# Kernel optimization log

Hardware: AMD Instinct MI355X
Metric: run time of the kernel (lower is better)

Reference implementation:

```python
import jax, jax.numpy as jnp
import numpy as np

DN = ('NCHW', 'OIHW', 'NCHW')
SCALES = (4, 2, 5, 2, 1914)  # per-feature one-hot widths; sum=1927, +1 scalar row = 1928 CNN channels


def conv(x, w, b, stride):
    y = jax.lax.conv_general_dilated(x, w, stride, 'VALID', dimension_numbers=DN)
    return y + b[None, :, None, None]


def maxpool(x, window):
    return jax.lax.reduce_window(x, -jnp.inf, jax.lax.max, (1, 1) + window, (1, 1) + window, 'VALID')


def setup_inputs() -> dict:
    key = jax.random.key(0)
    ks = jax.random.split(key, 16)
    B, T, F, H, W = 2, 32, 8, 128, 128
    replay = jax.random.randint(ks[0], (B, T, F, H, W), 0, 2).astype(jnp.float32)

    def rn(k, shape, scale=0.02):
        return jax.random.normal(k, shape, jnp.float32) * scale

    return dict(
        replay_tensor=replay,
        emb_table=rn(ks[1], (16384, 200), 1.0),
        conv_con_w=rn(ks[2], (1, 1, 4, 4)), conv_con_b=jnp.zeros((1,), jnp.float32),
        fc_con_w=rn(ks[3], (200, 961)), fc_con_b=jnp.zeros((200,), jnp.float32),
        cnn1_w=rn(ks[4], (964, 1928, 1, 2)), cnn1_b=jnp.zeros((964,), jnp.float32),
        cnn2_w=rn(ks[5], (482, 964, 1, 2)), cnn2_b=jnp.zeros((482,), jnp.float32),
        cnn3_w=rn(ks[6], (241, 482, 1, 2)), cnn3_b=jnp.zeros((241,), jnp.float32),
        cnn4_w=rn(ks[7], (100, 241, 1, 2)), cnn4_b=jnp.zeros((100,), jnp.float32),
        fc_cnn_w=rn(ks[8], (100, 2300)), fc_cnn_b=jnp.zeros((100,), jnp.float32),
        lstm_w_ih=rn(ks[9], (400, 100), 0.1), lstm_w_hh=rn(ks[10], (400, 100), 0.1),
        lstm_b_ih=jnp.zeros((400,), jnp.float32), lstm_b_hh=jnp.zeros((400,), jnp.float32),
        fc_out_w=rn(ks[11], (2, 100), 0.1), fc_out_b=jnp.zeros((2,), jnp.float32),
        batch_size=2,
    )


def reference(replay_tensor, emb_table, conv_con_w, conv_con_b, fc_con_w, fc_con_b,
              cnn1_w, cnn1_b, cnn2_w, cnn2_b, cnn3_w, cnn3_b, cnn4_w, cnn4_b,
              fc_cnn_w, fc_cnn_b, lstm_w_ih, lstm_w_hh, lstm_b_ih, lstm_b_hh,
              fc_out_w, fc_out_b, batch_size):
    # np.delete(replay, 2, 2) then np.delete(., 3, 2) removes original features 2 and 4
    replay = replay_tensor[:batch_size, :, jnp.array([0, 1, 3, 5, 6, 7])]
    B, T = replay.shape[0], replay.shape[1]
    scalar = replay[:, :, 0]   # [B,T,128,128]
    cat = replay[:, :, 1:6]    # [B,T,5,128,128]

    # --- categorical branch ---
    # The original builds a [scale_k, H*W] one-hot scatter per (b,t,k), then the
    # embedding step reads only spatial column 0: row s of the per-feature block is
    # emb_table[1] iff value_at_pos0 == s (nonzero after thresholding), else emb_table[0].
    v0 = cat[:, :, :, 0, 0].astype(jnp.int32)  # [B,T,5]
    embs = []
    for k, sc in enumerate(SCALES):
        v = v0[:, :, k]
        v = jnp.where(v > sc, 0, v)  # threshold: values > scale_ zeroed
        idx = ((jnp.arange(sc)[None, None, :] == v[:, :, None]) & (v[:, :, None] != 0)).astype(jnp.int32)
        embs.append(emb_table[idx])  # [B,T,sc,200]
    emb_full = jnp.concatenate(embs, axis=2)  # [B,T,1927,200]

    # --- scalar conv branch (faithful to the bug: cnn_con2 applied to raw x) ---
    x = scalar.reshape(B * T, 1, 128, 128)
    y = maxpool(jax.nn.relu(conv(x, conv_con_w, conv_con_b, (2, 2))), (2, 2))  # [BT,1,31,31]
    y = y.reshape(B * T, -1) @ fc_con_w.T + fc_con_b                           # [BT,200]
    sca_full = y.reshape(B, T, 1, 200)

    # --- CNN over concatenated [1928, 1, 200] frames ---
    z = jnp.concatenate([sca_full, emb_full], axis=2).reshape(B * T, 1928, 1, 200)
    z = maxpool(jax.nn.relu(conv(z, cnn1_w, cnn1_b, (1, 1))), (1, 2))
    z = maxpool(jax.nn.relu(conv(z, cnn2_w, cnn2_b, (1, 1))), (1, 2))
    z = maxpool(jax.nn.relu(conv(z, cnn3_w, cnn3_b, (1, 1))), (1, 2))
    z = jax.nn.relu(conv(z, cnn4_w, cnn4_b, (1, 1)))  # [BT,100,1,23]
    z = z.reshape(B * T, -1) @ fc_cnn_w.T + fc_cnn_b  # [BT,100]
    seq = z.reshape(B, T, 100)

    # --- single-layer LSTM (torch gate order i,f,g,o), zero init state ---
    def step(carry, x_t):
        h, c = carry
        g = x_t @ lstm_w_ih.T + h @ lstm_w_hh.T + lstm_b_ih + lstm_b_hh
        i, f, gg, o = jnp.split(g, 4, axis=-1)
        c = jax.nn.sigmoid(f) * c + jax.nn.sigmoid(i) * jnp.tanh(gg)
        h = jax.nn.sigmoid(o) * jnp.tanh(c)
        return (h, c), None

    h0 = jnp.zeros((B, 100), seq.dtype)
    c0 = jnp.zeros((B, 100), seq.dtype)
    (hT, _), _ = jax.lax.scan(step, (h0, c0), jnp.swapaxes(seq, 0, 1))
    return hT @ fc_out_w.T + fc_out_b  # [B,2]
```

## Files before the change

### kernel.cpp

```cpp
#include <hip/hip_runtime.h>
#include <math.h>

#define DEVFN __device__ __forceinline__

typedef __bf16 bf16x8 __attribute__((ext_vector_type(8)));
typedef float f32x4 __attribute__((ext_vector_type(4)));

constexpr int T_ = 32;
constexpr int HW = 128;
constexpr int C1IN = 1928;
constexpr int C1 = 964;

DEVFN float sigm(float x) { return 1.0f / (1.0f + __expf(-x)); }
DEVFN float tanhfast(float x) { return 2.0f / (1.0f + __expf(-2.0f * x)) - 1.0f; }

DEVFN ushort f2b(float v) {
    union { float f; unsigned u; } x; x.f = v;
    unsigned r = x.u + 0x7fffu + ((x.u >> 16) & 1u);
    return (ushort)(r >> 16);
}

DEVFN void gload16(const ushort* g, ushort* l) {
    __builtin_amdgcn_global_load_lds(
        (const __attribute__((address_space(1))) unsigned int*)g,
        (__attribute__((address_space(3))) unsigned int*)l, 16, 0, 0);
}

__global__ void k_sca_conv(const float* __restrict__ replay, const float* __restrict__ wc,
                           const float* __restrict__ bc, float* __restrict__ y) {
    const int n = blockIdx.x;
    const int idx = blockIdx.y * 256 + threadIdx.x;
    if (idx >= 961) return;
    const float* x = replay + (size_t)n * 8 * HW * HW;
    float wr_[16];
    #pragma unroll
    for (int t = 0; t < 16; ++t) wr_[t] = wc[t];
    const float bcv = bc[0];
    const int i = idx / 31, j = idx % 31;
    float m = 0.0f;
    #pragma unroll
    for (int di = 0; di < 2; ++di)
    #pragma unroll
    for (int dj = 0; dj < 2; ++dj) {
        const int h0 = 2 * (2 * i + di), w0 = 2 * (2 * j + dj);
        float acc = bcv;
        #pragma unroll
        for (int p = 0; p < 4; ++p)
        #pragma unroll
        for (int q = 0; q < 4; ++q)
            acc += x[(h0 + p) * HW + (w0 + q)] * wr_[p * 4 + q];
        m = fmaxf(m, fmaxf(acc, 0.0f));
    }
    y[n * 961 + idx] = m;
}

__global__ void k_sca_fc(const float* __restrict__ y, const float* __restrict__ fcw,
                         const float* __restrict__ fcb, float* __restrict__ sca) {
    const int n = blockIdx.x;
    const int wid = threadIdx.x >> 6, lane = threadIdx.x & 63;
    const int o = blockIdx.y * 4 + wid;
    float acc = 0.f;
    for (int m = lane; m < 961; m += 64)
        acc += y[n * 961 + m] * fcw[(size_t)o * 961 + m];
    #pragma unroll
    for (int off = 32; off > 0; off >>= 1) acc += __shfl_down(acc, off);
    if (lane == 0) sca[n * 200 + o] = acc + fcb[o];
}

__global__ void k_prep(const float* __restrict__ w1, const float* __restrict__ w2,
                       const float* __restrict__ w3, const float* __restrict__ w4,
                       const float* __restrict__ whh, const float* __restrict__ replay,
                       float* __restrict__ wsum, float* __restrict__ sa,
                       ushort* __restrict__ A2, ushort* __restrict__ A3,
                       ushort* __restrict__ A4, float* __restrict__ whhT) {
    const int bid = blockIdx.x;
    const int tx = threadIdx.x;
    constexpr int N2 = 2 * 512 * 1024;
    constexpr int N3 = 2 * 256 * 512;
    constexpr int N4 = 2 * 128 * 256;
    if (bid < 5533) {
        const int idx = bid * 256 + tx;
        if (idx < N2) {
            const int kw = idx >> 19;
            const int r = idx & 524287;
            const int oc = r >> 10, ic = r & 1023;
            const float v = (oc < 482 && ic < 964) ? w2[(size_t)oc * 1928 + ic * 2 + kw] : 0.f;
            A2[idx] = f2b(v);
        } else if (idx < N2 + N3) {
            const int j = idx - N2;
            const int kw = j >> 17;
            const int r = j & 131071;
            const int oc = r >> 9, ic = r & 511;
            const float v = (oc < 241 && ic < 482) ? w3[(size_t)oc * 964 + ic * 2 + kw] : 0.f;
            A3[j] = f2b(v);
        } else if (idx < N2 + N3 + N4) {
            const int j = idx - (N2 + N3);
            const int kw = j >> 15;
            const int r = j & 32767;
            const int oc = r >> 8, ic = r & 255;
            const float v = (oc < 100 && ic < 241) ? w4[(size_t)oc * 482 + ic * 2 + kw] : 0.f;
            A4[j] = f2b(v);
        } else {
            const int j = idx - (N2 + N3 + N4);
            if (j < 40000) {
                const int m = j / 400, p = j - m * 400;
                const int go = (p & 3) * 100 + (p >> 2);
                whhT[m * 400 + p] = whh[go * 100 + m];
            }
        }
    } else if (bid < 5774) {
        const int oc = (bid - 5533) * 4 + (tx >> 6);
        const int lane = tx & 63;
        const float* wr = w1 + (size_t)oc * C1IN * 2;
        float s0 = 0.f, s1 = 0.f;
        for (int ic = lane; ic < C1IN; ic += 64) {
            s0 += wr[ic * 2 + 0];
            s1 += wr[ic * 2 + 1];
        }
        #pragma unroll
        for (int off = 32; off > 0; off >>= 1) {
            s0 += __shfl_down(s0, off);
            s1 += __shfl_down(s1, off);
        }
        if (lane == 0) { wsum[oc * 2] = s0; wsum[oc * 2 + 1] = s1; }
    } else {
        const int j = bid - 5774;
        const int n = j >> 2;
        const int oc = (j & 3) * 256 + tx;
        if (oc < C1) {
            const int chs[5]    = {1, 3, 5, 6, 7};
            const int scales[5] = {4, 2, 5, 2, 1914};
            const int offs[5]   = {0, 4, 6, 11, 13};
            float s0 = 0.f, s1 = 0.f;
            #pragma unroll
            for (int k = 0; k < 5; ++k) {
                int v = (int)replay[((size_t)n * 8 + chs[k]) * HW * HW];
                if (v > scales[k]) v = 0;
                if (v >= 1 && v <= scales[k] - 1) {
                    const int ic = 1 + offs[k] + v;
                    s0 += w1[((size_t)oc * C1IN + ic) * 2 + 0];
                    s1 += w1[((size_t)oc * C1IN + ic) * 2 + 1];
                }
            }
            sa[(n * C1 + oc) * 2 + 0] = s0;
            sa[(n * C1 + oc) * 2 + 1] = s1;
        }
    }
}

template <int OCT>
__global__ void k_cnn1(const float* __restrict__ sca, const float* __restrict__ emb,
                       const float* __restrict__ w1, const float* __restrict__ b1,
                       const float* __restrict__ wsum, const float* __restrict__ sa,
                       ushort* __restrict__ Bt2) {
    const int n = blockIdx.x;
    const int ocBase = blockIdx.y * OCT;
    const int tx = threadIdx.x;
    __shared__ float ev[200], sv[200], dv[200];
    __shared__ float oscal[OCT][7];
    __shared__ float vals[OCT][100];
    for (int i = tx; i < 200; i += blockDim.x) {
        const float e0 = emb[i], e1 = emb[200 + i];
        ev[i] = e0;
        dv[i] = e1 - e0;
        sv[i] = sca[n * 200 + i] - e0;
    }
    for (int i = tx; i < OCT * 7; i += blockDim.x) {
        const int ocl = i / 7, f = i % 7;
        const int oc = ocBase + ocl;
        float v = 0.f;
        if (oc < C1) {
            switch (f) {
                case 0: v = wsum[oc * 2 + 0]; break;
                case 1: v = wsum[oc * 2 + 1]; break;
                case 2: v = b1[oc]; break;
                case 3: v = w1[(size_t)oc * C1IN * 2 + 0]; break;
                case 4: v = w1[(size_t)oc * C1IN * 2 + 1]; break;
                case 5: v = sa[(n * C1 + oc) * 2 + 0]; break;
                case 6: v = sa[(n * C1 + oc) * 2 + 1]; break;
            }
        }
        oscal[ocl][f] = v;
    }
    __syncthreads();
    for (int item = tx; item < OCT * 99; item += blockDim.x) {
        const int ocl = item / 99, u = item % 99;
        const int oc = ocBase + ocl;
        float res = 0.f;
        if (oc < C1) {
            const float ws0 = oscal[ocl][0], ws1 = oscal[ocl][1], bb = oscal[ocl][2];
            const float a0 = oscal[ocl][3], a1 = oscal[ocl][4];
            const float s0 = oscal[ocl][5], s1 = oscal[ocl][6];
            float r = -INFINITY;
            #pragma unroll
            for (int dw = 0; dw < 2; ++dw) {
                const int ww = 2 * u + dw;
                const float o = bb + ws0 * ev[ww] + ws1 * ev[ww + 1]
                                   + a0 * sv[ww] + a1 * sv[ww + 1]
                                   + s0 * dv[ww] + s1 * dv[ww + 1];
                r = fmaxf(r, o);
            }
            res = fmaxf(r, 0.0f);
        }
        vals[ocl][u] = res;
    }
    __syncthreads();
    for (int i = tx; i < OCT * 100; i += blockDim.x) {
        const int u = i >> 4, ocl = i & 15;
        const float v = (u < 99) ? vals[ocl][u] : 0.0f;
        Bt2[(size_t)(n * 100 + u) * 1024 + ocBase + ocl] = f2b(v);
    }
    if (n == 0 && ocBase == 0) {
        for (int i = tx; i < 1024; i += blockDim.x)
            Bt2[(size_t)6400 * 1024 + i] = 0;
    }
}

template <int OCREAL, int WR, int WOUT, int KICP, int MPAD, int OMODE, int OSTR,
          bool POOL, int MT, int NTILES>
__global__ __launch_bounds__(256, 2) void k_gemm_conv(
    const ushort* __restrict__ A, const ushort* __restrict__ Bt,
    const float* __restrict__ bias, void* __restrict__ outv) {
    constexpr int BK = 64;
    constexpr int NT = KICP / BK;
    constexpr int NWG = MT * NTILES;
    constexpr int Qq = NWG / 8, Rr = NWG % 8;

    __shared__ __align__(16) ushort As0[2][4096];
    __shared__ __align__(16) ushort As1[2][4096];
    __shared__ __align__(16) ushort Bs[2][8704];

    const int bid = blockIdx.x;
    const int xcd = bid & 7, rest = bid >> 3;
    const int base = (xcd < Rr) ? xcd * (Qq + 1) : Rr * (Qq + 1) + (xcd - Rr) * Qq;
    const int sid = base + rest;
    const int mBase = (sid % MT) * 64;
    const int nBase = (sid / MT) * 128;

    const int tx = threadIdx.x;
    const int wave = tx >> 6, lane = tx & 63;
    const int lr = lane & 15, lk = lane >> 4;
    const int r8 = lane >> 3;
    const int cx = (lane & 7) ^ r8;
    const ushort* A1p = A + (size_t)MPAD * KICP;

    f32x4 acc[4][2] = {};

    auto STAGE = [&](int buf, int kt) {
        const int k0 = kt * BK + cx * 8;
        #pragma unroll
        for (int it = 0; it < 2; ++it) {
            const int s = wave + it * 4;
            const int row = s * 8 + r8;
            gload16(&A[(size_t)(mBase + row) * KICP + k0], &As0[buf][s * 512]);
            gload16(&A1p[(size_t)(mBase + row) * KICP + k0], &As1[buf][s * 512]);
        }
        #pragma unroll
        for (int it = 0; it < 4; ++it) {
            const int s = wave + it * 4;
            const int row = s * 8 + r8;
            gload16(&Bt[(size_t)(nBase + row) * KICP + k0], &Bs[buf][s * 512]);
        }
        if (wave == 0) {
            const int row = 128 + r8;
            gload16(&Bt[(size_t)(nBase + row) * KICP + k0], &Bs[buf][16 * 512]);
        }
    };

    auto COMPUTE = [&](int cur) {
        #pragma unroll
        for (int ks = 0; ks < 2; ++ks) {
            bf16x8 a0[4], a1[4], b0[2], b1[2];
            #pragma unroll
            for (int i = 0; i < 4; ++i) {
                const int row = i * 16 + lr;
                const int col = (ks * 32 + lk * 8) ^ ((row & 7) << 3);
                a0[i] = *(const bf16x8*)&As0[cur][row * 64 + col];
                a1[i] = *(const bf16x8*)&As1[cur][row * 64 + col];
            }
            #pragma unroll
            for (int j = 0; j < 2; ++j) {
                const int row = wave * 32 + j * 16 + lr;
                const int col = (ks * 32 + lk * 8) ^ ((row & 7) << 3);
                b0[j] = *(const bf16x8*)&Bs[cur][row * 64 + col];
                const int row1 = row + 1;
                const int col1 = (ks * 32 + lk * 8) ^ ((row1 & 7) << 3);
                b1[j] = *(const bf16x8*)&Bs[cur][row1 * 64 + col1];
            }
            #pragma unroll
            for (int i = 0; i < 4; ++i)
                #pragma unroll
                for (int j = 0; j < 2; ++j) {
                    acc[i][j] = __builtin_amdgcn_mfma_f32_16x16x32_bf16(a0[i], b0[j], acc[i][j], 0, 0, 0);
                    acc[i][j] = __builtin_amdgcn_mfma_f32_16x16x32_bf16(a1[i], b1[j], acc[i][j], 0, 0, 0);
                }
        }
    };

    STAGE(0, 0);
    if (NT > 1) STAGE(1, 1);
    #pragma unroll 1
    for (int kt = 0; kt < NT; ++kt) {
        const int cur = kt & 1;
        if (kt + 1 < NT) {
            if (wave == 0) asm volatile("s_waitcnt vmcnt(9)" ::: "memory");
            else           asm volatile("s_waitcnt vmcnt(8)" ::: "memory");
        } else {
            asm volatile("s_waitcnt vmcnt(0)" ::: "memory");
        }
        __builtin_amdgcn_sched_barrier(0);
        __builtin_amdgcn_s_barrier();
        COMPUTE(cur);
        __builtin_amdgcn_s_barrier();
        if (kt + 2 < NT) STAGE(cur, kt + 2);
    }

    ushort* outb = (ushort*)outv;
    float*  outf = (float*)outv;
    constexpr int NOUTW = POOL ? (WOUT / 2) : WOUT;
    constexpr int WRN = NOUTW + 1;
    constexpr int NVALID = WR * 64;
    #pragma unroll
    for (int i = 0; i < 4; ++i) {
        const int m0 = mBase + i * 16 + lk * 4;
        #pragma unroll
        for (int j = 0; j < 2; ++j) {
            const int r = nBase + wave * 32 + j * 16 + lr;
            const int n = r / WR, w = r - n * WR;
            #pragma unroll
            for (int reg = 0; reg < 4; ++reg) {
                const float v = acc[i][j][reg];
                const float vo = __shfl_xor(v, 1);
                const int m = m0 + reg;
                const bool lok = POOL ? ((lr & 1) == 0) : true;
                if (lok && (w < WOUT) && (m < OCREAL) && (r < NVALID)) {
                    const float pre = POOL ? fmaxf(v, vo) : v;
                    const float val = fmaxf(pre + bias[m], 0.0f);
                    const int wc = POOL ? (w >> 1) : w;
                    if (OMODE == 2)
                        outb[((size_t)(n * WRN + wc)) * OSTR + m] = f2b(val);
                    else
                        outf[((size_t)n * OCREAL + m) * NOUTW + wc] = val;
                }
            }
        }
    }
}

__global__ void k_fc_cnn(const float* __restrict__ z4, const float* __restrict__ w,
                         const float* __restrict__ b, float* __restrict__ seq) {
    const int n = blockIdx.x;
    const int wid = threadIdx.x >> 6, lane = threadIdx.x & 63;
    const int o = blockIdx.y * 4 + wid;
    const float4* zr = (const float4*)(z4 + (size_t)n * 2300);
    const float4* wr = (const float4*)(w + (size_t)o * 2300);
    float acc = 0.f;
    for (int m = lane; m < 575; m += 64) {
        const float4 wv = wr[m];
        const float4 zv = zr[m];
        acc += wv.x * zv.x + wv.y * zv.y + wv.z * zv.z + wv.w * zv.w;
    }
    #pragma unroll
    for (int off = 32; off > 0; off >>= 1) acc += __shfl_down(acc, off);
    if (lane == 0) seq[n * 100 + o] = acc + b[o];
}

__global__ void k_xg(const float* __restrict__ seq, const float* __restrict__ wih,
                     const float* __restrict__ bih, const float* __restrict__ bhh,
                     float* __restrict__ xg) {
    const int n = blockIdx.x;
    __shared__ __align__(16) float s[100];
    if (threadIdx.x < 100) s[threadIdx.x] = seq[n * 100 + threadIdx.x];
    __syncthreads();
    const int p = threadIdx.x;
    if (p < 400) {
        const int go = (p & 3) * 100 + (p >> 2);
        const float4* wr = (const float4*)(wih + (size_t)go * 100);
        const float4* s4 = (const float4*)s;
        float4 a = {0.f, 0.f, 0.f, 0.f};
        #pragma unroll
        for (int m = 0; m < 25; ++m) {
            const float4 wv = wr[m];
            const float4 sv = s4[m];
            a.x += wv.x * sv.x; a.y += wv.y * sv.y;
            a.z += wv.z * sv.z; a.w += wv.w * sv.w;
        }
        xg[n * 400 + p] = bih[go] + bhh[go] + a.x + a.y + a.z + a.w;
    }
}

__global__ __launch_bounds__(448) void k_lstm(const float* __restrict__ xg,
                                              const float* __restrict__ whhT,
                                              const float* __restrict__ fw,
                                              const float* __restrict__ fb,
                                              float* __restrict__ outp) {
    const int bb = blockIdx.x;
    const int tx = threadIdx.x;
    __shared__ __align__(16) float hb[2][104];
    float wreg[100];
    if (tx < 400) {
        #pragma unroll
        for (int m = 0; m < 100; ++m) wreg[m] = whhT[m * 400 + tx];
    }
    float creg = 0.f;
    if (tx < 104) { hb[0][tx] = 0.f; hb[1][tx] = 0.f; }
    float xnext = (tx < 400) ? xg[(size_t)(bb * T_) * 400 + tx] : 0.f;
    __syncthreads();
    const int lane = tx & 63, base = lane & ~3;
    const int g = tx & 3;
    for (int t = 0; t < T_; ++t) {
        float act = 0.f;
        if (tx < 400) {
            float a0 = xnext, a1 = 0.f, a2 = 0.f, a3 = 0.f;
            if (t + 1 < T_) xnext = xg[(size_t)(bb * T_ + t + 1) * 400 + tx];
            const float4* h4 = (const float4*)&hb[t & 1][0];
            #pragma unroll
            for (int m4 = 0; m4 < 25; ++m4) {
                const float4 hv = h4[m4];
                a0 += hv.x * wreg[4 * m4 + 0];
                a1 += hv.y * wreg[4 * m4 + 1];
                a2 += hv.z * wreg[4 * m4 + 2];
                a3 += hv.w * wreg[4 * m4 + 3];
            }
            const float accv = (a0 + a1) + (a2 + a3);
            act = (g == 2) ? tanhfast(accv) : sigm(accv);
        }
        const float aI = __shfl(act, base + 0);
        const float aF = __shfl(act, base + 1);
        const float aG = __shfl(act, base + 2);
        const float aO = __shfl(act, base + 3);
        if (tx < 400) {
            const float cn = aF * creg + aI * aG;
            creg = cn;
            if (g == 0) hb[(t + 1) & 1][tx >> 2] = aO * tanhfast(cn);
        }
        __syncthreads();
    }
    if (tx < 2) {
        float acc = fb[tx];
        for (int j = 0; j < 100; ++j) acc += hb[0][j] * fw[tx * 100 + j];
        outp[bb * 2 + tx] = acc;
    }
}

extern "C" void kernel_launch(void* const* d_in, const int* in_sizes, int n_in,
                              void* d_out, int out_size, void* d_ws, size_t ws_size,
                              hipStream_t stream) {
    (void)in_sizes; (void)n_in; (void)out_size; (void)ws_size;
    const float* replay = (const float*)d_in[0];
    const float* emb    = (const float*)d_in[1];
    const float* ccw    = (const float*)d_in[2];
    const float* ccb    = (const float*)d_in[3];
    const float* fcw    = (const float*)d_in[4];
    const float* fcb    = (const float*)d_in[5];
    const float* w1     = (const float*)d_in[6];
    const float* b1     = (const float*)d_in[7];
    const float* w2     = (const float*)d_in[8];
    const float* b2     = (const float*)d_in[9];
    const float* w3     = (const float*)d_in[10];
    const float* b3     = (const float*)d_in[11];
    const float* w4     = (const float*)d_in[12];
    const float* b4     = (const float*)d_in[13];
    const float* fcnw   = (const float*)d_in[14];
    const float* fcnb   = (const float*)d_in[15];
    const float* wih    = (const float*)d_in[16];
    const float* whh    = (const float*)d_in[17];
    const float* bih    = (const float*)d_in[18];
    const float* bhh    = (const float*)d_in[19];
    const float* fow    = (const float*)d_in[20];
    const float* fob    = (const float*)d_in[21];

    float* ws = (float*)d_ws;
    float*  sca  = ws + 0;
    float*  wsum = ws + 12800;
    float*  sa   = ws + 14848;
    float*  seq  = ws + 138240;
    float*  xg   = ws + 144640;
    float*  whhT = ws + 170240;
    float*  yb   = ws + 210240;
    float*  z4   = ws + 272384;
    ushort* A2   = (ushort*)(ws + 419584);
    ushort* A3   = (ushort*)(ws + 943872);
    ushort* A4   = (ushort*)(ws + 1074944);
    ushort* Bt2  = (ushort*)(ws + 1107712);
    ushort* Bt3  = (ushort*)(ws + 4385024);
    ushort* Bt4  = (ushort*)(ws + 5208320);
    float*  outp = (float*)d_out;

    k_sca_conv<<<dim3(64, 4), 256, 0, stream>>>(replay, ccw, ccb, yb);
    k_sca_fc<<<dim3(64, 50), 256, 0, stream>>>(yb, fcw, fcb, sca);
    k_prep<<<6030, 256, 0, stream>>>(w1, w2, w3, w4, whh, replay,
                                     wsum, sa, A2, A3, A4, whhT);
    k_cnn1<16><<<dim3(64, 64), 256, 0, stream>>>(sca, emb, w1, b1, wsum, sa, Bt2);
    k_gemm_conv<482, 100, 98, 1024, 512, 2, 512, true, 8, 50>
        <<<400, 256, 0, stream>>>(A2, Bt2, b2, Bt3);
    k_gemm_conv<241, 50, 48, 512, 256, 2, 256, true, 4, 25>
        <<<100, 256, 0, stream>>>(A3, Bt3, b3, Bt4);
    k_gemm_conv<100, 25, 23, 256, 128, 0, 0, false, 2, 13>
        <<<26, 256, 0, stream>>>(A4, Bt4, b4, z4);
    k_fc_cnn<<<dim3(64, 25), 256, 0, stream>>>(z4, fcnw, fcnb, seq);
    k_xg<<<64, 512, 0, stream>>>(seq, wih, bih, bhh, xg);
    k_lstm<<<2, 448, 0, stream>>>(xg, whhT, fow, fob, outp);
}
```

Baseline: 140.7 us.

## Fuse small stage kernels into persistent kernels with software grid barriers

Merges the scalar conv into the prep kernel, fuses the scalar FC with the first CNN layer behind a grid-wide atomic barrier, and fuses conv3, conv4, the CNN FC and the LSTM input projection into one 128-block tail kernel with barriers between stages. The GEMM body becomes a device function with caller-provided shared buffers so it can be reused inside the fused kernel. This removes several kernel launches and their gaps. In exchange, the software barriers require every block to be co-resident, which risks deadlock, and the fused stages run with fixed grid sizes that may leave compute units idle.

```diff
diff --git a/kernel.cpp b/kernel.cpp
--- a/kernel.cpp
+++ b/kernel.cpp
@@ -26,60 +26,58 @@
         (__attribute__((address_space(3))) unsigned int*)l, 16, 0, 0);
 }
 
-__global__ void k_sca_conv(const float* __restrict__ replay, const float* __restrict__ wc,
-                           const float* __restrict__ bc, float* __restrict__ y) {
-    const int n = blockIdx.x;
-    const int idx = blockIdx.y * 256 + threadIdx.x;
-    if (idx >= 961) return;
-    const float* x = replay + (size_t)n * 8 * HW * HW;
-    float wr_[16];
-    #pragma unroll
-    for (int t = 0; t < 16; ++t) wr_[t] = wc[t];
-    const float bcv = bc[0];
-    const int i = idx / 31, j = idx % 31;
-    float m = 0.0f;
-    #pragma unroll
-    for (int di = 0; di < 2; ++di)
-    #pragma unroll
-    for (int dj = 0; dj < 2; ++dj) {
-        const int h0 = 2 * (2 * i + di), w0 = 2 * (2 * j + dj);
-        float acc = bcv;
-        #pragma unroll
-        for (int p = 0; p < 4; ++p)
-        #pragma unroll
-        for (int q = 0; q < 4; ++q)
-            acc += x[(h0 + p) * HW + (w0 + q)] * wr_[p * 4 + q];
-        m = fmaxf(m, fmaxf(acc, 0.0f));
-    }
-    y[n * 961 + idx] = m;
-}
-
-__global__ void k_sca_fc(const float* __restrict__ y, const float* __restrict__ fcw,
-                         const float* __restrict__ fcb, float* __restrict__ sca) {
-    const int n = blockIdx.x;
-    const int wid = threadIdx.x >> 6, lane = threadIdx.x & 63;
-    const int o = blockIdx.y * 4 + wid;
-    float acc = 0.f;
-    for (int m = lane; m < 961; m += 64)
-        acc += y[n * 961 + m] * fcw[(size_t)o * 961 + m];
-    #pragma unroll
-    for (int off = 32; off > 0; off >>= 1) acc += __shfl_down(acc, off);
-    if (lane == 0) sca[n * 200 + o] = acc + fcb[o];
-}
-
-__global__ void k_prep(const float* __restrict__ w1, const float* __restrict__ w2,
-                       const float* __restrict__ w3, const float* __restrict__ w4,
-                       const float* __restrict__ whh, const float* __restrict__ replay,
-                       float* __restrict__ wsum, float* __restrict__ sa,
-                       ushort* __restrict__ A2, ushort* __restrict__ A3,
-                       ushort* __restrict__ A4, float* __restrict__ whhT) {
+DEVFN void gbar(int* c, int target) {
+    __syncthreads();
+    if (threadIdx.x == 0) {
+        __threadfence();
+        __hip_atomic_fetch_add(c, 1, __ATOMIC_RELEASE, __HIP_MEMORY_SCOPE_AGENT);
+        while (__hip_atomic_load(c, __ATOMIC_ACQUIRE, __HIP_MEMORY_SCOPE_AGENT) < target)
+            __builtin_amdgcn_s_sleep(2);
+        __threadfence();
+    }
+    __syncthreads();
+}
+
+__global__ void k_front(const float* __restrict__ replay, const float* __restrict__ wc,
+                        const float* __restrict__ bc, const float* __restrict__ w1,
+                        const float* __restrict__ w2, const float* __restrict__ w3,
+                        const float* __restrict__ w4, const float* __restrict__ whh,
+                        float* __restrict__ yb, float* __restrict__ wsum,
+                        float* __restrict__ sa, ushort* __restrict__ A2,
+                        ushort* __restrict__ A3, ushort* __restrict__ A4,
+                        float* __restrict__ whhT, int* __restrict__ bars) {
     const int bid = blockIdx.x;
     const int tx = threadIdx.x;
     constexpr int N2 = 2 * 512 * 1024;
     constexpr int N3 = 2 * 256 * 512;
     constexpr int N4 = 2 * 128 * 256;
-    if (bid < 5533) {
-        const int idx = bid * 256 + tx;
+    if (bid < 256) {
+        const int n = bid >> 2;
+        const int idx = (bid & 3) * 256 + tx;
+        if (idx >= 961) return;
+        const float* x = replay + (size_t)n * 8 * HW * HW;
+        float wr_[16];
+        #pragma unroll
+        for (int t = 0; t < 16; ++t) wr_[t] = wc[t];
+        const float bcv = bc[0];
+        const int i = idx / 31, j = idx % 31;
+        float m = 0.0f;
+        #pragma unroll
+        for (int di = 0; di < 2; ++di)
+        #pragma unroll
+        for (int dj = 0; dj < 2; ++dj) {
+            const int h0 = 2 * (2 * i + di), w0 = 2 * (2 * j + dj);
+            float acc = bcv;
+            #pragma unroll
+            for (int p = 0; p < 4; ++p)
+            #pragma unroll
+            for (int q = 0; q < 4; ++q)
+                acc += x[(h0 + p) * HW + (w0 + q)] * wr_[p * 4 + q];
+            m = fmaxf(m, fmaxf(acc, 0.0f));
+        }
+        yb[n * 961 + idx] = m;
+    } else if (bid < 256 + 5533) {
+        const int idx = (bid - 256) * 256 + tx;
         if (idx < N2) {
             const int kw = idx >> 19;
             const int r = idx & 524287;
@@ -108,8 +106,8 @@
                 whhT[m * 400 + p] = whh[go * 100 + m];
             }
         }
-    } else if (bid < 5774) {
-        const int oc = (bid - 5533) * 4 + (tx >> 6);
+    } else if (bid < 256 + 5774) {
+        const int oc = (bid - (256 + 5533)) * 4 + (tx >> 6);
         const int lane = tx & 63;
         const float* wr = w1 + (size_t)oc * C1IN * 2;
         float s0 = 0.f, s1 = 0.f;
@@ -123,8 +121,8 @@
             s1 += __shfl_down(s1, off);
         }
         if (lane == 0) { wsum[oc * 2] = s0; wsum[oc * 2 + 1] = s1; }
-    } else {
-        const int j = bid - 5774;
+    } else if (bid < 256 + 6030) {
+        const int j = bid - (256 + 5774);
         const int n = j >> 2;
         const int oc = (j & 3) * 256 + tx;
         if (oc < C1) {
@@ -145,95 +143,105 @@
             sa[(n * C1 + oc) * 2 + 0] = s0;
             sa[(n * C1 + oc) * 2 + 1] = s1;
         }
-    }
-}
-
-template <int OCT>
-__global__ void k_cnn1(const float* __restrict__ sca, const float* __restrict__ emb,
-                       const float* __restrict__ w1, const float* __restrict__ b1,
-                       const float* __restrict__ wsum, const float* __restrict__ sa,
-                       ushort* __restrict__ Bt2) {
-    const int n = blockIdx.x;
-    const int ocBase = blockIdx.y * OCT;
+    } else {
+        if (tx < 16) bars[tx] = 0;
+    }
+}
+
+__global__ __launch_bounds__(256, 4) void k_mid(
+    const float* __restrict__ yb, const float* __restrict__ fcw,
+    const float* __restrict__ fcb, float* __restrict__ sca,
+    const float* __restrict__ emb, const float* __restrict__ w1,
+    const float* __restrict__ b1, const float* __restrict__ wsum,
+    const float* __restrict__ sa, ushort* __restrict__ Bt2,
+    int* __restrict__ bars) {
+    const int bid = blockIdx.x;
     const int tx = threadIdx.x;
+    const int wid = tx >> 6, lane = tx & 63;
     __shared__ float ev[200], sv[200], dv[200];
-    __shared__ float oscal[OCT][7];
-    __shared__ float vals[OCT][100];
-    for (int i = tx; i < 200; i += blockDim.x) {
-        const float e0 = emb[i], e1 = emb[200 + i];
-        ev[i] = e0;
-        dv[i] = e1 - e0;
-        sv[i] = sca[n * 200 + i] - e0;
-    }
-    for (int i = tx; i < OCT * 7; i += blockDim.x) {
-        const int ocl = i / 7, f = i % 7;
-        const int oc = ocBase + ocl;
-        float v = 0.f;
-        if (oc < C1) {
-            switch (f) {
-                case 0: v = wsum[oc * 2 + 0]; break;
-                case 1: v = wsum[oc * 2 + 1]; break;
-                case 2: v = b1[oc]; break;
-                case 3: v = w1[(size_t)oc * C1IN * 2 + 0]; break;
-                case 4: v = w1[(size_t)oc * C1IN * 2 + 1]; break;
-                case 5: v = sa[(n * C1 + oc) * 2 + 0]; break;
-                case 6: v = sa[(n * C1 + oc) * 2 + 1]; break;
-            }
-        }
-        oscal[ocl][f] = v;
-    }
-    __syncthreads();
-    for (int item = tx; item < OCT * 99; item += blockDim.x) {
-        const int ocl = item / 99, u = item % 99;
-        const int oc = ocBase + ocl;
-        float res = 0.f;
-        if (oc < C1) {
-            const float ws0 = oscal[ocl][0], ws1 = oscal[ocl][1], bb = oscal[ocl][2];
-            const float a0 = oscal[ocl][3], a1 = oscal[ocl][4];
-            const float s0 = oscal[ocl][5], s1 = oscal[ocl][6];
-            float r = -INFINITY;
-            #pragma unroll
-            for (int dw = 0; dw < 2; ++dw) {
-                const int ww = 2 * u + dw;
-                const float o = bb + ws0 * ev[ww] + ws1 * ev[ww + 1]
-                                   + a0 * sv[ww] + a1 * sv[ww + 1]
-                                   + s0 * dv[ww] + s1 * dv[ww + 1];
-                r = fmaxf(r, o);
-            }
-            res = fmaxf(r, 0.0f);
-        }
-        vals[ocl][u] = res;
-    }
-    __syncthreads();
-    for (int i = tx; i < OCT * 100; i += blockDim.x) {
-        const int u = i >> 4, ocl = i & 15;
-        const float v = (u < 99) ? vals[ocl][u] : 0.0f;
-        Bt2[(size_t)(n * 100 + u) * 1024 + ocBase + ocl] = f2b(v);
-    }
-    if (n == 0 && ocBase == 0) {
-        for (int i = tx; i < 1024; i += blockDim.x)
-            Bt2[(size_t)6400 * 1024 + i] = 0;
+    __shared__ float oscal[16][7];
+    __shared__ float vals[16][100];
+
+    for (int t = bid * 4 + wid; t < 12800; t += 4096) {
+        const int n = t / 200, o = t % 200;
+        float acc = 0.f;
+        for (int m = lane; m < 961; m += 64)
+            acc += yb[n * 961 + m] * fcw[(size_t)o * 961 + m];
+        #pragma unroll
+        for (int off = 32; off > 0; off >>= 1) acc += __shfl_down(acc, off);
+        if (lane == 0) sca[n * 200 + o] = acc + fcb[o];
+    }
+    gbar(&bars[0], 1024);
+
+    for (int tk = bid; tk < 4096; tk += 1024) {
+        const int n = tk >> 6;
+        const int ocBase = (tk & 63) * 16;
+        for (int i = tx; i < 200; i += 256) {
+            const float e0 = emb[i], e1 = emb[200 + i];
+            ev[i] = e0;
+            dv[i] = e1 - e0;
+            sv[i] = sca[n * 200 + i] - e0;
+        }
+        for (int i = tx; i < 16 * 7; i += 256) {
+            const int ocl = i / 7, f = i % 7;
+            const int oc = ocBase + ocl;
+            float v = 0.f;
+            if (oc < C1) {
+                switch (f) {
+                    case 0: v = wsum[oc * 2 + 0]; break;
+                    case 1: v = wsum[oc * 2 + 1]; break;
+                    case 2: v = b1[oc]; break;
+                    case 3: v = w1[(size_t)oc * C1IN * 2 + 0]; break;
+                    case 4: v = w1[(size_t)oc * C1IN * 2 + 1]; break;
+                    case 5: v = sa[(n * C1 + oc) * 2 + 0]; break;
+                    case 6: v = sa[(n * C1 + oc) * 2 + 1]; break;
+                }
+            }
+            oscal[ocl][f] = v;
+        }
+        __syncthreads();
+        for (int item = tx; item < 16 * 99; item += 256) {
+            const int ocl = item / 99, u = item % 99;
+            const int oc = ocBase + ocl;
+            float res = 0.f;
+            if (oc < C1) {
+                const float ws0 = oscal[ocl][0], ws1 = oscal[ocl][1], bb = oscal[ocl][2];
+                const float a0 = oscal[ocl][3], a1 = oscal[ocl][4];
+                const float s0 = oscal[ocl][5], s1 = oscal[ocl][6];
+                float r = -INFINITY;
+                #pragma unroll
+                for (int dw = 0; dw < 2; ++dw) {
+                    const int ww = 2 * u + dw;
+                    const float o = bb + ws0 * ev[ww] + ws1 * ev[ww + 1]
+                                       + a0 * sv[ww] + a1 * sv[ww + 1]
+                                       + s0 * dv[ww] + s1 * dv[ww + 1];
+                    r = fmaxf(r, o);
+                }
+                res = fmaxf(r, 0.0f);
+            }
+            vals[ocl][u] = res;
+        }
+        __syncthreads();
+        for (int i = tx; i < 16 * 100; i += 256) {
+            const int u = i >> 4, ocl = i & 15;
+            const float v = (u < 99) ? vals[ocl][u] : 0.0f;
+            Bt2[(size_t)(n * 100 + u) * 1024 + ocBase + ocl] = f2b(v);
+        }
+        if (tk == 0) {
+            for (int i = tx; i < 1024; i += 256)
+                Bt2[(size_t)6400 * 1024 + i] = 0;
+        }
+        __syncthreads();
     }
 }
 
 template <int OCREAL, int WR, int WOUT, int KICP, int MPAD, int OMODE, int OSTR,
-          bool POOL, int MT, int NTILES>
-__global__ __launch_bounds__(256, 2) void k_gemm_conv(
-    const ushort* __restrict__ A, const ushort* __restrict__ Bt,
-    const float* __restrict__ bias, void* __restrict__ outv) {
+          bool POOL, int MT>
+DEVFN void gemm_body(int sid, const ushort* __restrict__ A,
+                     const ushort* __restrict__ Bt, const float* __restrict__ bias,
+                     void* __restrict__ outv, ushort* As0, ushort* As1, ushort* Bs) {
     constexpr int BK = 64;
     constexpr int NT = KICP / BK;
-    constexpr int NWG = MT * NTILES;
-    constexpr int Qq = NWG / 8, Rr = NWG % 8;
-
-    __shared__ __align__(16) ushort As0[2][4096];
-    __shared__ __align__(16) ushort As1[2][4096];
-    __shared__ __align__(16) ushort Bs[2][8704];
-
-    const int bid = blockIdx.x;
-    const int xcd = bid & 7, rest = bid >> 3;
-    const int base = (xcd < Rr) ? xcd * (Qq + 1) : Rr * (Qq + 1) + (xcd - Rr) * Qq;
-    const int sid = base + rest;
     const int mBase = (sid % MT) * 64;
     const int nBase = (sid / MT) * 128;
 
@@ -252,18 +260,18 @@
         for (int it = 0; it < 2; ++it) {
             const int s = wave + it * 4;
             const int row = s * 8 + r8;
-            gload16(&A[(size_t)(mBase + row) * KICP + k0], &As0[buf][s * 512]);
-            gload16(&A1p[(size_t)(mBase + row) * KICP + k0], &As1[buf][s * 512]);
+            gload16(&A[(size_t)(mBase + row) * KICP + k0], &As0[buf * 4096 + s * 512]);
+            gload16(&A1p[(size_t)(mBase + row) * KICP + k0], &As1[buf * 4096 + s * 512]);
         }
         #pragma unroll
         for (int it = 0; it < 4; ++it) {
             const int s = wave + it * 4;
             const int row = s * 8 + r8;
-            gload16(&Bt[(size_t)(nBase + row) * KICP + k0], &Bs[buf][s * 512]);
+            gload16(&Bt[(size_t)(nBase + row) * KICP + k0], &Bs[buf * 8704 + s * 512]);
         }
         if (wave == 0) {
             const int row = 128 + r8;
-            gload16(&Bt[(size_t)(nBase + row) * KICP + k0], &Bs[buf][16 * 512]);
+            gload16(&Bt[(size_t)(nBase + row) * KICP + k0], &Bs[buf * 8704 + 16 * 512]);
         }
     };
 
@@ -275,17 +283,17 @@
             for (int i = 0; i < 4; ++i) {
                 const int row = i * 16 + lr;
                 const int col = (ks * 32 + lk * 8) ^ ((row & 7) << 3);
-                a0[i] = *(const bf16x8*)&As0[cur][row * 64 + col];
-                a1[i] = *(const bf16x8*)&As1[cur][row * 64 + col];
+                a0[i] = *(const bf16x8*)&As0[cur * 4096 + row * 64 + col];
+                a1[i] = *(const bf16x8*)&As1[cur * 4096 + row * 64 + col];
             }
             #pragma unroll
             for (int j = 0; j < 2; ++j) {
                 const int row = wave * 32 + j * 16 + lr;
                 const int col = (ks * 32 + lk * 8) ^ ((row & 7) << 3);
-                b0[j] = *(const bf16x8*)&Bs[cur][row * 64 + col];
+                b0[j] = *(const bf16x8*)&Bs[cur * 8704 + row * 64 + col];
                 const int row1 = row + 1;
                 const int col1 = (ks * 32 + lk * 8) ^ ((row1 & 7) << 3);
-                b1[j] = *(const bf16x8*)&Bs[cur][row1 * 64 + col1];
+                b1[j] = *(const bf16x8*)&Bs[cur * 8704 + row1 * 64 + col1];
             }
             #pragma unroll
             for (int i = 0; i < 4; ++i)
@@ -347,36 +355,68 @@
     }
 }
 
-__global__ void k_fc_cnn(const float* __restrict__ z4, const float* __restrict__ w,
-                         const float* __restrict__ b, float* __restrict__ seq) {
-    const int n = blockIdx.x;
-    const int wid = threadIdx.x >> 6, lane = threadIdx.x & 63;
-    const int o = blockIdx.y * 4 + wid;
-    const float4* zr = (const float4*)(z4 + (size_t)n * 2300);
-    const float4* wr = (const float4*)(w + (size_t)o * 2300);
-    float acc = 0.f;
-    for (int m = lane; m < 575; m += 64) {
-        const float4 wv = wr[m];
-        const float4 zv = zr[m];
-        acc += wv.x * zv.x + wv.y * zv.y + wv.z * zv.z + wv.w * zv.w;
-    }
-    #pragma unroll
-    for (int off = 32; off > 0; off >>= 1) acc += __shfl_down(acc, off);
-    if (lane == 0) seq[n * 100 + o] = acc + b[o];
-}
-
-__global__ void k_xg(const float* __restrict__ seq, const float* __restrict__ wih,
-                     const float* __restrict__ bih, const float* __restrict__ bhh,
-                     float* __restrict__ xg) {
-    const int n = blockIdx.x;
-    __shared__ __align__(16) float s[100];
-    if (threadIdx.x < 100) s[threadIdx.x] = seq[n * 100 + threadIdx.x];
-    __syncthreads();
-    const int p = threadIdx.x;
-    if (p < 400) {
+template <int OCREAL, int WR, int WOUT, int KICP, int MPAD, int OMODE, int OSTR,
+          bool POOL, int MT, int NTILES>
+__global__ __launch_bounds__(256, 2) void k_gemm_conv(
+    const ushort* __restrict__ A, const ushort* __restrict__ Bt,
+    const float* __restrict__ bias, void* __restrict__ outv) {
+    __shared__ __align__(16) ushort As0[8192];
+    __shared__ __align__(16) ushort As1[8192];
+    __shared__ __align__(16) ushort Bs[17408];
+    constexpr int NWG = MT * NTILES;
+    constexpr int Qq = NWG / 8, Rr = NWG % 8;
+    const int bid = blockIdx.x;
+    const int xcd = bid & 7, rest = bid >> 3;
+    const int base = (xcd < Rr) ? xcd * (Qq + 1) : Rr * (Qq + 1) + (xcd - Rr) * Qq;
+    const int sid = base + rest;
+    gemm_body<OCREAL, WR, WOUT, KICP, MPAD, OMODE, OSTR, POOL, MT>(
+        sid, A, Bt, bias, outv, As0, As1, Bs);
+}
+
+__global__ __launch_bounds__(256, 2) void k_tail(
+    const ushort* __restrict__ A3, const ushort* __restrict__ Bt3,
+    const float* __restrict__ b3, ushort* __restrict__ Bt4,
+    const ushort* __restrict__ A4, const float* __restrict__ b4,
+    float* __restrict__ z4, const float* __restrict__ fcnw,
+    const float* __restrict__ fcnb, float* __restrict__ seq,
+    const float* __restrict__ wih, const float* __restrict__ bih,
+    const float* __restrict__ bhh, float* __restrict__ xg,
+    int* __restrict__ bars) {
+    __shared__ __align__(16) ushort As0[8192];
+    __shared__ __align__(16) ushort As1[8192];
+    __shared__ __align__(16) ushort Bs[17408];
+    const int bid = blockIdx.x;
+    const int tx = threadIdx.x;
+    if (bid < 100)
+        gemm_body<241, 50, 48, 512, 256, 2, 256, true, 4>(
+            bid, A3, Bt3, b3, Bt4, As0, As1, Bs);
+    gbar(&bars[1], 128);
+    if (bid < 26)
+        gemm_body<100, 25, 23, 256, 128, 0, 0, false, 2>(
+            bid, A4, Bt4, b4, z4, As0, As1, Bs);
+    gbar(&bars[2], 128);
+    const int wid = tx >> 6, lane = tx & 63;
+    for (int t = bid * 4 + wid; t < 6400; t += 512) {
+        const int n = t / 100, o = t % 100;
+        const float4* zr = (const float4*)(z4 + (size_t)n * 2300);
+        const float4* wr = (const float4*)(fcnw + (size_t)o * 2300);
+        float acc = 0.f;
+        for (int m = lane; m < 575; m += 64) {
+            const float4 wv = wr[m];
+            const float4 zv = zr[m];
+            acc += wv.x * zv.x + wv.y * zv.y + wv.z * zv.z + wv.w * zv.w;
+        }
+        #pragma unroll
+        for (int off = 32; off > 0; off >>= 1) acc += __shfl_down(acc, off);
+        if (lane == 0) seq[n * 100 + o] = acc + fcnb[o];
+    }
+    gbar(&bars[3], 128);
+    const int idx = bid * 256 + tx;
+    if (idx < 25600) {
+        const int n = idx / 400, p = idx - (idx / 400) * 400;
         const int go = (p & 3) * 100 + (p >> 2);
         const float4* wr = (const float4*)(wih + (size_t)go * 100);
-        const float4* s4 = (const float4*)s;
+        const float4* s4 = (const float4*)(seq + (size_t)n * 100);
         float4 a = {0.f, 0.f, 0.f, 0.f};
         #pragma unroll
         for (int m = 0; m < 25; ++m) {
@@ -477,7 +517,8 @@
     float*  seq  = ws + 138240;
     float*  xg   = ws + 144640;
     float*  whhT = ws + 170240;
-    float*  yb   = ws + 210240;
+    int*    bars = (int*)(ws + 210240);
+    float*  yb   = ws + 210432;
     float*  z4   = ws + 272384;
     ushort* A2   = (ushort*)(ws + 419584);
     ushort* A3   = (ushort*)(ws + 943872);
@@ -487,18 +528,13 @@
     ushort* Bt4  = (ushort*)(ws + 5208320);
     float*  outp = (float*)d_out;
 
-    k_sca_conv<<<dim3(64, 4), 256, 0, stream>>>(replay, ccw, ccb, yb);
-    k_sca_fc<<<dim3(64, 50), 256, 0, stream>>>(yb, fcw, fcb, sca);
-    k_prep<<<6030, 256, 0, stream>>>(w1, w2, w3, w4, whh, replay,
-                                     wsum, sa, A2, A3, A4, whhT);
-    k_cnn1<16><<<dim3(64, 64), 256, 0, stream>>>(sca, emb, w1, b1, wsum, sa, Bt2);
+    k_front<<<6287, 256, 0, stream>>>(replay, ccw, ccb, w1, w2, w3, w4, whh,
+                                      yb, wsum, sa, A2, A3, A4, whhT, bars);
+    k_mid<<<1024, 256, 0, stream>>>(yb, fcw, fcb, sca, emb, w1, b1, wsum, sa,
+                                    Bt2, bars);
     k_gemm_conv<482, 100, 98, 1024, 512, 2, 512, true, 8, 50>
         <<<400, 256, 0, stream>>>(A2, Bt2, b2, Bt3);
-    k_gemm_conv<241, 50, 48, 512, 256, 2, 256, true, 4, 25>
-        <<<100, 256, 0, stream>>>(A3, Bt3, b3, Bt4);
-    k_gemm_conv<100, 25, 23, 256, 128, 0, 0, false, 2, 13>
-        <<<26, 256, 0, stream>>>(A4, Bt4, b4, z4);
-    k_fc_cnn<<<dim3(64, 25), 256, 0, stream>>>(z4, fcnw, fcnb, seq);
-    k_xg<<<64, 512, 0, stream>>>(seq, wih, bih, bhh, xg);
+    k_tail<<<128, 256, 0, stream>>>(A3, Bt3, b3, Bt4, A4, b4, z4,
+                                    fcnw, fcnb, seq, wih, bih, bhh, xg, bars);
     k_lstm<<<2, 448, 0, stream>>>(xg, whhT, fow, fob, outp);
 }
```

Measured after the change: 420.3 us. +198.8%, slower.
